# Performance work log

Measured on AMD Instinct MI355X. Metric: run time of the kernel, lower is better.

The kernel has to match this reference:

```python
import jax, jax.numpy as jnp
import numpy as np

B, L, V, E = 4096, 200, 100000, 50  # users, max ratings per user, movie vocab, embedding size


def setup_inputs() -> dict:
    key = jax.random.key(0)
    ks = jax.random.split(key, 10)
    emb = jax.random.normal(ks[0], (V, E), jnp.float32) * 0.1
    user_movie_idx = jax.random.randint(ks[1], (B, L), 0, V)
    lengths = jax.random.randint(ks[2], (B,), 1, L + 1)  # at least 1 rating per user
    ratings = jax.random.uniform(ks[3], (B, L), jnp.float32, 0.5, 5.0)
    movie_idx = jax.random.randint(ks[4], (B,), 0, V)

    def lin(k, fan_in, fan_out):
        bound = 1.0 / np.sqrt(fan_in)
        return jax.random.uniform(k, (fan_in, fan_out), jnp.float32, -bound, bound)

    W1 = lin(ks[5], 5 * E, 2 * E)
    b1 = jnp.zeros((2 * E,), jnp.float32)
    W2 = lin(ks[6], 2 * E, E)
    b2 = jnp.zeros((E,), jnp.float32)
    W3 = lin(ks[7], E, 1)
    b3 = jnp.zeros((1,), jnp.float32)
    return dict(emb=emb, ratings=ratings, W1=W1, b1=b1, W2=W2, b2=b2, W3=W3, b3=b3,
                user_movie_idx=user_movie_idx, lengths=lengths, movie_idx=movie_idx)


def reference(emb, ratings, W1, b1, W2, b2, W3, b3, user_movie_idx, lengths, movie_idx):
    # ragged per-user weighted gather: [B, L, E]
    mask = (jnp.arange(L)[None, :] < lengths[:, None])  # [B, L] valid positions
    w = emb[user_movie_idx] * ratings[:, :, None]
    m = mask[:, :, None]
    inf = jnp.float32(jnp.inf)

    wmin = jnp.min(jnp.where(m, w, inf), axis=1)          # [B, E]
    wmax = jnp.max(jnp.where(m, w, -inf), axis=1)         # [B, E]
    n = lengths[:, None].astype(w.dtype)
    wmean = jnp.sum(jnp.where(m, w, 0.0), axis=1) / n     # [B, E]
    # torch median = lower median: sorted index (n-1)//2; pad with +inf so it sorts last
    ws = jnp.sort(jnp.where(m, w, inf), axis=1)
    med_idx = jnp.broadcast_to(((lengths - 1) // 2)[:, None, None], (B, 1, E))
    wmed = jnp.take_along_axis(ws, med_idx, axis=1)[:, 0, :]  # [B, E]

    u = jnp.concatenate([wmin, wmax, wmean, wmed], axis=1)  # [B, 4E]
    u = u / jnp.linalg.norm(u, axis=1, keepdims=True)

    x = jnp.concatenate([u, emb[movie_idx]], axis=1)        # [B, 5E]
    h = jax.nn.relu(x @ W1 + b1)   # dropout is identity in eval
    h = jax.nn.relu(h @ W2 + b2)
    return jax.nn.sigmoid(h @ W3 + b3)  # [B, 1]
```

## Files before the change

### kernel.cpp

```cpp
#include <hip/hip_runtime.h>
#include <math.h>

#define NB 4096
#define LL 200
#define EE 50
#define CH 104
#define CP 105
#define NT 512
#define GG 8
#define IT 25
#define IT1 13
#define SW 8

#define K2B 256
#define K2T 512
#define BPB 16

__device__ __forceinline__ unsigned f2key(float f) {
    unsigned b = __float_as_uint(f);
    unsigned mask = (b & 0x80000000u) ? 0xFFFFFFFFu : 0x80000000u;
    return b ^ mask;
}
__device__ __forceinline__ float key2f(unsigned kk) {
    unsigned mask = (kk & 0x80000000u) ? 0x80000000u : 0xFFFFFFFFu;
    return __uint_as_float(kk ^ mask);
}

__device__ __forceinline__ unsigned select_median(
    int n, int k, int g, int grp, const unsigned it[IT],
    unsigned kmin, unsigned kmax, unsigned (*sbuf)[SW], int *scnt)
{
    unsigned LO = kmin, HI = kmax + 1u;
    int cLO = 0, cHI = n;
    unsigned med = 0u;
    bool small = false;
    int pass = 0;
    for (;;) {
        if (HI - LO == 1u) { med = LO; break; }
        const int w = cHI - cLO;
        if (w <= SW) { small = true; break; }
        unsigned P;
        if (pass < 8) {
            const float vlo = key2f(LO);
            const float vhi = key2f(HI - 1u);
            const float frac = (float)(k - cLO + 1) / (float)(w + 1);
            P = f2key(vlo + (vhi - vlo) * frac);
        } else {
            P = LO + ((HI - LO) >> 1);
        }
        if (P <= LO) P = LO + 1u;
        if (P >= HI) P = HI - 1u;
        int c = 0;
        #pragma unroll
        for (int t = 0; t < IT; t++) c += (it[t] < P) ? 1 : 0;
        c += __shfl_xor(c, 1);
        c += __shfl_xor(c, 2);
        c += __shfl_xor(c, 4);
        if (c > k) { HI = P; cHI = c; }
        else       { LO = P; cLO = c; }
        pass++;
    }
    if (small) {
        const int w = cHI - cLO;
        const int r = k - cLO;
        #pragma unroll
        for (int t = 0; t < IT; t++) {
            const unsigned kk = it[t];
            if (kk >= LO && kk < HI) {
                const int pos = atomicAdd(&scnt[grp], 1);
                if (pos < SW) sbuf[grp][pos] = kk;
            }
        }
        const unsigned sv = (g < w) ? sbuf[grp][g] : 0xFFFFFFFFu;
        int cLess = 0, cLeq = 0;
        for (int j = 0; j < w; j++) {
            const unsigned o = sbuf[grp][j];
            cLess += (o <  sv) ? 1 : 0;
            cLeq  += (o <= sv) ? 1 : 0;
        }
        unsigned cand = (g < w && cLess <= r && r < cLeq) ? sv : 0xFFFFFFFFu;
        #pragma unroll
        for (int m2 = 1; m2 < GG; m2 <<= 1)
            cand = min(cand, (unsigned)__shfl_xor((int)cand, m2));
        med = cand;
    }
    return med;
}

extern "C" __global__ void __launch_bounds__(NT, 8)
rec_stats(const float* __restrict__ emb, const float* __restrict__ ratings,
          const int* __restrict__ uidx, const int* __restrict__ lens,
          float* __restrict__ uo)
{
    __shared__ unsigned wK[EE][CP];
    __shared__ int      idxL[LL];
    __shared__ float    ratL[LL];
    __shared__ unsigned sbuf[EE][SW];
    __shared__ int      scnt[EE];

    const int b   = blockIdx.x;
    const int tid = threadIdx.x;
    const int n   = lens[b];
    const int k   = (n - 1) >> 1;

    if (tid < EE) scnt[tid] = 0;
    if (tid < n) {
        idxL[tid] = uidx[b*LL + tid];
        ratL[tid] = ratings[b*LL + tid];
    }
    __syncthreads();

    const int f = tid >> 3;
    const int g = tid & 7;

    const int c1 = (n < CH) ? n : CH;
    for (int p = tid; p < c1*(EE/2); p += NT) {
        const int l  = p / (EE/2);
        const int e2 = p - l*(EE/2);
        const float2 ev = ((const float2*)emb)[(size_t)idxL[l]*(EE/2) + e2];
        const float  r  = ratL[l];
        wK[2*e2    ][l] = f2key(ev.x * r);
        wK[2*e2 + 1][l] = f2key(ev.y * r);
    }
    __syncthreads();

    unsigned it[IT];
    unsigned kmin = 0xFFFFFFFFu, kmax = 0u;
    float sm = 0.f;
    if (f < EE) {
        #pragma unroll
        for (int t = 0; t < IT1; t++) {
            const int l = g + (t << 3);
            unsigned kk = 0xFFFFFFFFu;
            if (l < n) {
                kk = wK[f][l];
                kmin = min(kmin, kk); kmax = max(kmax, kk); sm += key2f(kk);
            }
            it[t] = kk;
        }
    }
    __syncthreads();

    const int c2 = n - CH;
    for (int p = tid; p < c2*(EE/2); p += NT) {
        const int col = p / (EE/2);
        const int e2  = p - col*(EE/2);
        const int l   = CH + col;
        const float2 ev = ((const float2*)emb)[(size_t)idxL[l]*(EE/2) + e2];
        const float  r  = ratL[l];
        wK[2*e2    ][col] = f2key(ev.x * r);
        wK[2*e2 + 1][col] = f2key(ev.y * r);
    }
    __syncthreads();

    if (f < EE) {
        #pragma unroll
        for (int t = IT1; t < IT; t++) {
            const int l = g + (t << 3);
            unsigned kk = 0xFFFFFFFFu;
            if (l < n) {
                kk = wK[f][l - CH];
                kmin = min(kmin, kk); kmax = max(kmax, kk); sm += key2f(kk);
            }
            it[t] = kk;
        }
        #pragma unroll
        for (int m2 = 1; m2 < GG; m2 <<= 1) {
            kmin = min(kmin, (unsigned)__shfl_xor((int)kmin, m2));
            kmax = max(kmax, (unsigned)__shfl_xor((int)kmax, m2));
            sm  += __shfl_xor(sm, m2);
        }

        const unsigned med = select_median(n, k, g, f, it, kmin, kmax,
                                           sbuf, scnt);
        if (g == 0) {
            float* ub = uo + (size_t)b * (4*EE);
            ub[f]        = key2f(kmin);
            ub[EE + f]   = key2f(kmax);
            ub[2*EE + f] = sm / (float)n;
            ub[3*EE + f] = key2f(med);
        }
    }
}

extern "C" __global__ void __launch_bounds__(K2T, 2)
rec_mlp(const float* __restrict__ emb,
        const float* __restrict__ W1, const float* __restrict__ b1,
        const float* __restrict__ W2, const float* __restrict__ b2,
        const float* __restrict__ W3, const float* __restrict__ b3,
        const int* __restrict__ midx, const float* __restrict__ uo,
        float* __restrict__ out)
{
    __shared__ float W1s[5*EE * 2*EE];
    __shared__ float W2s[2*EE * EE];
    __shared__ float b1s[2*EE];
    __shared__ float b2s[EE];
    __shared__ float W3s[EE];
    __shared__ float xs[8][252];

    const int tid = threadIdx.x;

    for (int p = tid; p < (5*EE*2*EE)/2; p += K2T)
        ((float2*)W1s)[p] = ((const float2*)W1)[p];
    for (int p = tid; p < (2*EE*EE)/2; p += K2T)
        ((float2*)W2s)[p] = ((const float2*)W2)[p];
    if (tid < 2*EE) b1s[tid] = b1[tid];
    if (tid < EE)   { b2s[tid] = b2[tid]; W3s[tid] = W3[tid]; }
    __syncthreads();
    const float bias3 = b3[0];

    const int w    = tid >> 6;
    const int lane = tid & 63;

    #pragma unroll
    for (int rep = 0; rep < 2; rep++) {
        const int b = blockIdx.x * BPB + rep * 8 + w;

        float uv0 = 0.f, uv1 = 0.f, uv2 = 0.f, uv3 = 0.f;
        const float* ub = uo + (size_t)b * (4*EE);
        uv0 = ub[lane];
        uv1 = ub[lane + 64];
        uv2 = ub[lane + 128];
        if (lane < 4*EE - 192) uv3 = ub[lane + 192];
        float v2 = uv0*uv0 + uv1*uv1 + uv2*uv2 + uv3*uv3;
        #pragma unroll
        for (int m2 = 1; m2 < 64; m2 <<= 1) v2 += __shfl_xor(v2, m2);
        const float inv = 1.0f / sqrtf(v2);

        xs[w][lane]       = uv0 * inv;
        xs[w][lane + 64]  = uv1 * inv;
        xs[w][lane + 128] = uv2 * inv;
        if (lane < 4*EE - 192) xs[w][lane + 192] = uv3 * inv;
        if (lane < EE) xs[w][4*EE + lane] = emb[(size_t)midx[b]*EE + lane];
        asm volatile("s_waitcnt lgkmcnt(0)" ::: "memory");

        const int o2 = (lane + 64 < 2*EE) ? lane + 64 : 2*EE - 1;
        float a0 = 0.f, a1 = 0.f;
        #pragma unroll 5
        for (int i = 0; i < 5*EE; i++) {
            const float xv = xs[w][i];
            a0 += xv * W1s[i*(2*EE) + lane];
            a1 += xv * W1s[i*(2*EE) + o2];
        }
        const float h0  = fmaxf(a0 + b1s[lane], 0.f);
        const float h64 = fmaxf(a1 + b1s[o2],   0.f);
        xs[w][lane] = h0;
        if (lane < 2*EE - 64) xs[w][lane + 64] = h64;
        asm volatile("s_waitcnt lgkmcnt(0)" ::: "memory");

        const int oc = (lane < EE) ? lane : EE - 1;
        float a2 = 0.f;
        #pragma unroll 5
        for (int i = 0; i < 2*EE; i++)
            a2 += xs[w][i] * W2s[i*EE + oc];
        const float h2v = fmaxf(a2 + b2s[oc], 0.f);
        float v = (lane < EE) ? h2v * W3s[lane] : 0.f;
        #pragma unroll
        for (int m2 = 1; m2 < 64; m2 <<= 1) v += __shfl_xor(v, m2);
        if (lane == 0) out[b] = 1.0f / (1.0f + expf(-(v + bias3)));
    }
}

extern "C" void kernel_launch(void* const* d_in, const int* in_sizes, int n_in,
                              void* d_out, int out_size, void* d_ws, size_t ws_size,
                              hipStream_t stream) {
    const float* emb     = (const float*)d_in[0];
    const float* ratings = (const float*)d_in[1];
    const float* W1      = (const float*)d_in[2];
    const float* b1      = (const float*)d_in[3];
    const float* W2      = (const float*)d_in[4];
    const float* b2      = (const float*)d_in[5];
    const float* W3      = (const float*)d_in[6];
    const float* b3      = (const float*)d_in[7];
    const int*   uidx    = (const int*)d_in[8];
    const int*   lens    = (const int*)d_in[9];
    const int*   midx    = (const int*)d_in[10];
    float* out = (float*)d_out;
    float* uo  = (float*)d_ws;

    hipLaunchKernelGGL(rec_stats, dim3(NB), dim3(NT), 0, stream,
                       emb, ratings, uidx, lens, uo);
    hipLaunchKernelGGL(rec_mlp, dim3(K2B), dim3(K2T), 0, stream,
                       emb, W1, b1, W2, b2, W3, b3, midx, uo, out);
}
```

Measured before the change: 93.46 us.

## Use 1024-thread blocks with full-length LDS tile and 16-lane median groups

The stats kernel now stores the whole 200-element weighted row per feature in shared memory, which removes the two-phase chunked gather and its extra barriers. It doubles the block size to 1024 threads so each feature is handled by a 16-lane group holding 13 values per lane, and adds a shuffle step to the median count reduction. The gather loop is rewritten with 1000 threads striding over rows. Larger LDS use (about 40KB) and larger blocks may reduce the number of resident blocks per CU, and the launch bounds value of 8 may not be valid for 1024 threads.

```diff
diff --git a/kernel.cpp b/kernel.cpp
--- a/kernel.cpp
+++ b/kernel.cpp
@@ -4,12 +4,10 @@
 #define NB 4096
 #define LL 200
 #define EE 50
-#define CH 104
-#define CP 105
-#define NT 512
-#define GG 8
-#define IT 25
-#define IT1 13
+#define LP 201
+#define NT 1024
+#define GG 16
+#define IT 13
 #define SW 8
 
 #define K2B 256
@@ -56,6 +54,7 @@
         c += __shfl_xor(c, 1);
         c += __shfl_xor(c, 2);
         c += __shfl_xor(c, 4);
+        c += __shfl_xor(c, 8);
         if (c > k) { HI = P; cHI = c; }
         else       { LO = P; cLO = c; }
         pass++;
@@ -92,75 +91,52 @@
           const int* __restrict__ uidx, const int* __restrict__ lens,
           float* __restrict__ uo)
 {
-    __shared__ unsigned wK[EE][CP];
+    __shared__ unsigned wK[EE][LP];
     __shared__ int      idxL[LL];
     __shared__ float    ratL[LL];
-    __shared__ unsigned sbuf[EE][SW];
-    __shared__ int      scnt[EE];
+    __shared__ unsigned sbuf[NT/GG][SW];
+    __shared__ int      scnt[NT/GG];
 
     const int b   = blockIdx.x;
     const int tid = threadIdx.x;
     const int n   = lens[b];
     const int k   = (n - 1) >> 1;
 
-    if (tid < EE) scnt[tid] = 0;
+    if (tid < NT/GG) scnt[tid] = 0;
     if (tid < n) {
         idxL[tid] = uidx[b*LL + tid];
         ratL[tid] = ratings[b*LL + tid];
     }
     __syncthreads();
 
-    const int f = tid >> 3;
-    const int g = tid & 7;
-
-    const int c1 = (n < CH) ? n : CH;
-    for (int p = tid; p < c1*(EE/2); p += NT) {
-        const int l  = p / (EE/2);
-        const int e2 = p - l*(EE/2);
-        const float2 ev = ((const float2*)emb)[(size_t)idxL[l]*(EE/2) + e2];
-        const float  r  = ratL[l];
-        wK[2*e2    ][l] = f2key(ev.x * r);
-        wK[2*e2 + 1][l] = f2key(ev.y * r);
+    if (tid < 40 * (EE/2)) {
+        const int e2 = tid % (EE/2);
+        int l        = tid / (EE/2);
+        for (; l < n; l += 40) {
+            const float2 ev = ((const float2*)emb)[(size_t)idxL[l]*(EE/2) + e2];
+            const float  r  = ratL[l];
+            wK[2*e2    ][l] = f2key(ev.x * r);
+            wK[2*e2 + 1][l] = f2key(ev.y * r);
+        }
     }
     __syncthreads();
 
-    unsigned it[IT];
-    unsigned kmin = 0xFFFFFFFFu, kmax = 0u;
-    float sm = 0.f;
+    const int f = tid >> 4;
+    const int g = tid & 15;
+
     if (f < EE) {
-        #pragma unroll
-        for (int t = 0; t < IT1; t++) {
-            const int l = g + (t << 3);
+        unsigned it[IT];
+        unsigned kmin = 0xFFFFFFFFu, kmax = 0u;
+        float sm = 0.f;
+        #pragma unroll
+        for (int t = 0; t < IT; t++) {
+            const int l = g + (t << 4);
             unsigned kk = 0xFFFFFFFFu;
             if (l < n) {
                 kk = wK[f][l];
-                kmin = min(kmin, kk); kmax = max(kmax, kk); sm += key2f(kk);
-            }
-            it[t] = kk;
-        }
-    }
-    __syncthreads();
-
-    const int c2 = n - CH;
-    for (int p = tid; p < c2*(EE/2); p += NT) {
-        const int col = p / (EE/2);
-        const int e2  = p - col*(EE/2);
-        const int l   = CH + col;
-        const float2 ev = ((const float2*)emb)[(size_t)idxL[l]*(EE/2) + e2];
-        const float  r  = ratL[l];
-        wK[2*e2    ][col] = f2key(ev.x * r);
-        wK[2*e2 + 1][col] = f2key(ev.y * r);
-    }
-    __syncthreads();
-
-    if (f < EE) {
-        #pragma unroll
-        for (int t = IT1; t < IT; t++) {
-            const int l = g + (t << 3);
-            unsigned kk = 0xFFFFFFFFu;
-            if (l < n) {
-                kk = wK[f][l - CH];
-                kmin = min(kmin, kk); kmax = max(kmax, kk); sm += key2f(kk);
+                kmin = min(kmin, kk);
+                kmax = max(kmax, kk);
+                sm += key2f(kk);
             }
             it[t] = kk;
         }
```

Result: slower. 111.2 us (+18.9%).

## Fuse per-user stats and MLP into a single kernel

Applied to the files above, without the earlier changes.

Merges the stats kernel and the MLP kernel into one launch: each block keeps its user's min/max/mean/median vector in shared memory, then one wavefront runs the normalization and the three-layer MLP, reading W1/W2 straight from global memory. This drops the second launch and the workspace round trip. In exchange, the MLP runs serially in a single wave per block while the other 448 threads idle, and every block re-reads the ~100KB of weights through cache rather than staging them once in LDS.

```diff
diff --git a/kernel.cpp b/kernel.cpp
--- a/kernel.cpp
+++ b/kernel.cpp
@@ -11,10 +11,6 @@
 #define IT 25
 #define IT1 13
 #define SW 8
-
-#define K2B 256
-#define K2T 512
-#define BPB 16
 
 __device__ __forceinline__ unsigned f2key(float f) {
     unsigned b = __float_as_uint(f);
@@ -88,22 +84,28 @@
 }
 
 extern "C" __global__ void __launch_bounds__(NT, 8)
-rec_stats(const float* __restrict__ emb, const float* __restrict__ ratings,
+rec_fused(const float* __restrict__ emb, const float* __restrict__ ratings,
+          const float* __restrict__ W1, const float* __restrict__ b1,
+          const float* __restrict__ W2, const float* __restrict__ b2,
+          const float* __restrict__ W3, const float* __restrict__ b3,
           const int* __restrict__ uidx, const int* __restrict__ lens,
-          float* __restrict__ uo)
+          const int* __restrict__ midx, float* __restrict__ out)
 {
     __shared__ unsigned wK[EE][CP];
     __shared__ int      idxL[LL];
     __shared__ float    ratL[LL];
-    __shared__ unsigned sbuf[EE][SW];
-    __shared__ int      scnt[EE];
+    __shared__ unsigned sbuf[NT/GG][SW];
+    __shared__ int      scnt[NT/GG];
+    __shared__ float    u[4*EE];
+    __shared__ float    xs[5*EE];
+    __shared__ float    h1s[2*EE];
 
     const int b   = blockIdx.x;
     const int tid = threadIdx.x;
     const int n   = lens[b];
     const int k   = (n - 1) >> 1;
 
-    if (tid < EE) scnt[tid] = 0;
+    if (tid < NT/GG) scnt[tid] = 0;
     if (tid < n) {
         idxL[tid] = uidx[b*LL + tid];
         ratL[tid] = ratings[b*LL + tid];
@@ -174,90 +176,57 @@
         const unsigned med = select_median(n, k, g, f, it, kmin, kmax,
                                            sbuf, scnt);
         if (g == 0) {
-            float* ub = uo + (size_t)b * (4*EE);
-            ub[f]        = key2f(kmin);
-            ub[EE + f]   = key2f(kmax);
-            ub[2*EE + f] = sm / (float)n;
-            ub[3*EE + f] = key2f(med);
-        }
-    }
-}
-
-extern "C" __global__ void __launch_bounds__(K2T, 2)
-rec_mlp(const float* __restrict__ emb,
-        const float* __restrict__ W1, const float* __restrict__ b1,
-        const float* __restrict__ W2, const float* __restrict__ b2,
-        const float* __restrict__ W3, const float* __restrict__ b3,
-        const int* __restrict__ midx, const float* __restrict__ uo,
-        float* __restrict__ out)
-{
-    __shared__ float W1s[5*EE * 2*EE];
-    __shared__ float W2s[2*EE * EE];
-    __shared__ float b1s[2*EE];
-    __shared__ float b2s[EE];
-    __shared__ float W3s[EE];
-    __shared__ float xs[8][252];
-
-    const int tid = threadIdx.x;
-
-    for (int p = tid; p < (5*EE*2*EE)/2; p += K2T)
-        ((float2*)W1s)[p] = ((const float2*)W1)[p];
-    for (int p = tid; p < (2*EE*EE)/2; p += K2T)
-        ((float2*)W2s)[p] = ((const float2*)W2)[p];
-    if (tid < 2*EE) b1s[tid] = b1[tid];
-    if (tid < EE)   { b2s[tid] = b2[tid]; W3s[tid] = W3[tid]; }
-    __syncthreads();
-    const float bias3 = b3[0];
-
-    const int w    = tid >> 6;
-    const int lane = tid & 63;
-
-    #pragma unroll
-    for (int rep = 0; rep < 2; rep++) {
-        const int b = blockIdx.x * BPB + rep * 8 + w;
-
-        float uv0 = 0.f, uv1 = 0.f, uv2 = 0.f, uv3 = 0.f;
-        const float* ub = uo + (size_t)b * (4*EE);
-        uv0 = ub[lane];
-        uv1 = ub[lane + 64];
-        uv2 = ub[lane + 128];
-        if (lane < 4*EE - 192) uv3 = ub[lane + 192];
+            u[f]        = key2f(kmin);
+            u[EE + f]   = key2f(kmax);
+            u[2*EE + f] = sm / (float)n;
+            u[3*EE + f] = key2f(med);
+        }
+    }
+    __syncthreads();
+
+    if (tid < 64) {
+        const int lane = tid;
+
+        const float uv0 = u[lane];
+        const float uv1 = u[lane + 64];
+        const float uv2 = u[lane + 128];
+        const float uv3 = (lane < 4*EE - 192) ? u[lane + 192] : 0.f;
         float v2 = uv0*uv0 + uv1*uv1 + uv2*uv2 + uv3*uv3;
         #pragma unroll
         for (int m2 = 1; m2 < 64; m2 <<= 1) v2 += __shfl_xor(v2, m2);
         const float inv = 1.0f / sqrtf(v2);
 
-        xs[w][lane]       = uv0 * inv;
-        xs[w][lane + 64]  = uv1 * inv;
-        xs[w][lane + 128] = uv2 * inv;
-        if (lane < 4*EE - 192) xs[w][lane + 192] = uv3 * inv;
-        if (lane < EE) xs[w][4*EE + lane] = emb[(size_t)midx[b]*EE + lane];
+        xs[lane]       = uv0 * inv;
+        xs[lane + 64]  = uv1 * inv;
+        xs[lane + 128] = uv2 * inv;
+        if (lane < 4*EE - 192) xs[lane + 192] = uv3 * inv;
+        if (lane < EE) xs[4*EE + lane] = emb[(size_t)midx[b]*EE + lane];
         asm volatile("s_waitcnt lgkmcnt(0)" ::: "memory");
 
         const int o2 = (lane + 64 < 2*EE) ? lane + 64 : 2*EE - 1;
         float a0 = 0.f, a1 = 0.f;
         #pragma unroll 5
         for (int i = 0; i < 5*EE; i++) {
-            const float xv = xs[w][i];
-            a0 += xv * W1s[i*(2*EE) + lane];
-            a1 += xv * W1s[i*(2*EE) + o2];
-        }
-        const float h0  = fmaxf(a0 + b1s[lane], 0.f);
-        const float h64 = fmaxf(a1 + b1s[o2],   0.f);
-        xs[w][lane] = h0;
-        if (lane < 2*EE - 64) xs[w][lane + 64] = h64;
+            const float xv = xs[i];
+            a0 += xv * W1[i*(2*EE) + lane];
+            a1 += xv * W1[i*(2*EE) + o2];
+        }
+        const float h0  = fmaxf(a0 + b1[lane], 0.f);
+        const float h64 = fmaxf(a1 + b1[o2],   0.f);
+        h1s[lane] = h0;
+        if (lane < 2*EE - 64) h1s[lane + 64] = h64;
         asm volatile("s_waitcnt lgkmcnt(0)" ::: "memory");
 
         const int oc = (lane < EE) ? lane : EE - 1;
         float a2 = 0.f;
         #pragma unroll 5
         for (int i = 0; i < 2*EE; i++)
-            a2 += xs[w][i] * W2s[i*EE + oc];
-        const float h2v = fmaxf(a2 + b2s[oc], 0.f);
-        float v = (lane < EE) ? h2v * W3s[lane] : 0.f;
+            a2 += h1s[i] * W2[i*EE + oc];
+        const float h2v = fmaxf(a2 + b2[oc], 0.f);
+        float v = (lane < EE) ? h2v * W3[lane] : 0.f;
         #pragma unroll
         for (int m2 = 1; m2 < 64; m2 <<= 1) v += __shfl_xor(v, m2);
-        if (lane == 0) out[b] = 1.0f / (1.0f + expf(-(v + bias3)));
+        if (lane == 0) out[b] = 1.0f / (1.0f + expf(-(v + b3[0])));
     }
 }
 
@@ -276,10 +245,7 @@
     const int*   lens    = (const int*)d_in[9];
     const int*   midx    = (const int*)d_in[10];
     float* out = (float*)d_out;
-    float* uo  = (float*)d_ws;
-
-    hipLaunchKernelGGL(rec_stats, dim3(NB), dim3(NT), 0, stream,
-                       emb, ratings, uidx, lens, uo);
-    hipLaunchKernelGGL(rec_mlp, dim3(K2B), dim3(K2T), 0, stream,
-                       emb, W1, b1, W2, b2, W3, b3, midx, uo, out);
-}
+
+    hipLaunchKernelGGL(rec_fused, dim3(NB), dim3(NT), 0, stream,
+                       emb, ratings, W1, b1, W2, b2, W3, b3, uidx, lens, midx, out);
+}
```

Result: slower. 103.3 us (+10.6%).
